# Optimization experiments

Measured on AMD Instinct MI355X. Metric: run time of the kernel, lower is better.

Reference implementation:

```python
import jax, jax.numpy as jnp
import numpy as np

N_WORDS = 8192   # total words across all concepts
L = 24           # chars per word (padded)
D = 256          # word_vec_d
H = 8            # attention heads
DFF = 1024
VOCAB = 128
N_CONCEPTS = 1024
MAXW = 16        # max_words
GROUPS = 4       # n_names: 4 equal groups of concepts


def setup_inputs() -> dict:
    key = jax.random.key(0)
    ks = jax.random.split(key, 9)
    rng = np.random.default_rng(0)
    # char tokens in [1, VOCAB), ragged word lengths in [4, L], tail = 0 (pad)
    vals = rng.integers(1, VOCAB, size=(N_WORDS, L))
    lens = rng.integers(4, L + 1, size=(N_WORDS,))
    inputs = np.where(np.arange(L)[None, :] < lens[:, None], vals, 0)
    # ragged words-per-concept: alternate 4 / 12 -> sums to N_WORDS, <= MAXW
    counts = np.where(np.arange(N_CONCEPTS) % 2 == 0, 4, 12)
    concept_id = np.repeat(np.arange(N_CONCEPTS), counts)
    word_pos = np.concatenate([np.arange(c) for c in counts])

    def w(k, shape):
        return 0.02 * jax.random.normal(k, shape, jnp.float32)

    return {
        "inputs": jnp.asarray(inputs, jnp.int32),
        "concept_id": jnp.asarray(concept_id, jnp.int32),
        "word_pos": jnp.asarray(word_pos, jnp.int32),
        "n_concepts": N_CONCEPTS,
        "n_names": GROUPS,
        "we_emb": w(ks[0], (VOCAB, D)),
        "we_qkv": w(ks[1], (D, 3 * D)),
        "we_o": w(ks[2], (D, D)),
        "we_ff1": w(ks[3], (D, DFF)),
        "we_ff2": w(ks[4], (DFF, D)),
        "ne_qkv": w(ks[5], (D, 3 * D)),
        "ne_o": w(ks[6], (D, D)),
        "ne_ff1": w(ks[7], (D, DFF)),
        "ne_ff2": w(ks[8], (DFF, D)),
    }


def _ln(x):
    m = x.mean(-1, keepdims=True)
    v = ((x - m) ** 2).mean(-1, keepdims=True)
    return (x - m) * jax.lax.rsqrt(v + 1e-5)


def _mha(x, wqkv, wo, key_pad=None):
    n, l, d = x.shape
    hd = d // H
    q, k, v = jnp.split(x @ wqkv, 3, axis=-1)
    q = q.reshape(n, l, H, hd)
    k = k.reshape(n, l, H, hd)
    v = v.reshape(n, l, H, hd)
    s = jnp.einsum('nqhd,nkhd->nhqk', q, k) / jnp.sqrt(jnp.asarray(hd, x.dtype))
    if key_pad is not None:
        s = jnp.where(key_pad[:, None, None, :], -1e9, s)
    a = jax.nn.softmax(s, axis=-1)
    o = jnp.einsum('nhqk,nkhd->nqhd', a, v).reshape(n, l, d)
    return o @ wo


def _block(x, wqkv, wo, w1, w2, key_pad=None):
    h = _ln(x + _mha(x, wqkv, wo, key_pad))
    return _ln(h + jax.nn.relu(h @ w1) @ w2)


def reference(inputs, concept_id, word_pos, n_concepts, n_names,
              we_emb, we_qkv, we_o, we_ff1, we_ff2,
              ne_qkv, ne_o, ne_ff1, ne_ff2):
    pad_mask = inputs == 0  # [N_WORDS, L]
    x = we_emb[inputs]      # [N_WORDS, L, D]
    word_ft = _block(x, we_qkv, we_o, we_ff1, we_ff2, pad_mask)
    # masked mean over chars -> one vector per word
    np_mask = (~pad_mask)[..., None].astype(word_ft.dtype)  # [N_WORDS, L, 1]
    name_vec = (word_ft * np_mask).sum(1) / np_mask.sum(1)   # [N_WORDS, D]
    # ragged -> padded: one scatter instead of per-sample torch.cat
    padded = jnp.zeros((n_concepts, MAXW, name_vec.shape[-1]), name_vec.dtype)
    padded = padded.at[concept_id, word_pos].set(name_vec)   # [n_concepts, MAXW, D]
    name_ft = _block(padded, ne_qkv, ne_o, ne_ff1, ne_ff2)
    row_pad = (padded == 0).all(-1, keepdims=True)           # all-zero rows = pad words
    name_ft = jnp.where(row_pad, jnp.zeros((), name_ft.dtype), name_ft)
    counts = (name_ft != 0).sum(1).astype(name_ft.dtype)     # [n_concepts, D]
    pooled = name_ft.sum(1) / counts                         # [n_concepts, D]
    return tuple(jnp.split(pooled, n_names, axis=0))
```

## Files before the change

### kernel.cpp

```cpp
#include <hip/hip_runtime.h>
#include <hip/hip_bf16.h>

#define NWORDS 8192
#define LW 24
#define DIM 256
#define NHEAD 8
#define DFF 1024
#define NCONC 1024
#define MAXW 16
#define TN (NCONC * MAXW)

typedef float floatx4 __attribute__((ext_vector_type(4)));
typedef short shortx8 __attribute__((ext_vector_type(8)));

__device__ __forceinline__ float bf2f(ushort u) {
  union { uint u; float f; } v; v.u = ((uint)u) << 16; return v.f;
}
__device__ __forceinline__ ushort f2bf(float f) {
  union { float f; uint u; } v; v.f = f;
  return (ushort)((v.u + 0x7FFFu + ((v.u >> 16) & 1u)) >> 16);
}

__device__ __forceinline__ void load_lds16(const ushort* gsrc, ushort* lds) {
  __builtin_amdgcn_global_load_lds((const __attribute__((address_space(1))) void*)gsrc,
                                   (__attribute__((address_space(3))) void*)lds, 16, 0, 0);
}

#define WAIT_VM0() __builtin_amdgcn_s_waitcnt(0x0F70)
#define WAIT_LGKM0() __builtin_amdgcn_s_waitcnt(0xC07F)

#define STAGE_COL(lane) ((((lane) & 3) ^ (((lane) >> 3) & 3)) * 8)
#define FRAG_OFF(row, quad) (((row) * 32) + ((((quad) ^ (((row) >> 1) & 3))) * 8))

__global__ __launch_bounds__(256) void wprep(const float* __restrict__ W,
                                             ushort* __restrict__ WT, int K, int N) {
  int idx = blockIdx.x * 256 + threadIdx.x;
  if (idx < K * N) {
    int k = idx / N, n = idx % N;
    WT[n * K + k] = f2bf(W[idx]);
  }
}

__global__ __launch_bounds__(256) void embed4(const int* __restrict__ inputs,
                                              const float* __restrict__ we_emb,
                                              ushort* __restrict__ x, int ntok) {
  int idx = blockIdx.x * 256 + threadIdx.x;
  int t = idx >> 6, d = (idx & 63) * 4;
  if (t < ntok) {
    const float4 f = *(const float4*)&we_emb[inputs[t] * DIM + d];
    uint2 o;
    o.x = (uint)f2bf(f.x) | ((uint)f2bf(f.y) << 16);
    o.y = (uint)f2bf(f.z) | ((uint)f2bf(f.w) << 16);
    *(uint2*)&x[(size_t)t * DIM + d] = o;
  }
}

template <bool LN>
__global__ __launch_bounds__(256, 2) void gemm_tok64(const ushort* __restrict__ A, int lda,
                                                     const ushort* __restrict__ BT,
                                                     const ushort* __restrict__ RES,
                                                     ushort* __restrict__ C, int ldc) {
  __shared__ __align__(16) ushort As[8 * 64 * 32];
  __shared__ __align__(16) ushort Wb[256 * 32];
  __shared__ float red1[64 * 4];
  __shared__ float red2[64 * 4];
  const int tid = threadIdx.x;
  const int w = tid >> 6, lane = tid & 63;
  const int quad = lane >> 4, l16 = lane & 15;
  const long m0 = (long)blockIdx.y * 64;
  const long nb = (long)blockIdx.x * 256;
  const int srow = lane >> 2;
  const int scol = STAGE_COL(lane);
  const int wc = w * 64;

#pragma unroll
  for (int t = 0; t < 8; t++) {
    int p = 2 * w + t / 4, ii = t % 4;
    load_lds16(&A[(m0 + ii * 16 + srow) * lda + p * 32 + scol], &As[p * 2048 + (ii * 16) * 32]);
  }
#pragma unroll
  for (int ii = 0; ii < 4; ii++)
    load_lds16(&BT[(nb + wc + ii * 16 + srow) * 256 + scol], &Wb[(wc + ii * 16) * 32]);
  __syncthreads();

  floatx4 acc[4][4] = {};
#pragma unroll 1
  for (int p = 0; p < 8; p++) {
    WAIT_VM0();
    shortx8 a[4], b[4];
#pragma unroll
    for (int j = 0; j < 4; j++)
      b[j] = *(const shortx8*)&Wb[FRAG_OFF(wc + j * 16 + l16, quad)];
    WAIT_LGKM0();
    if (p < 7) {
#pragma unroll
      for (int ii = 0; ii < 4; ii++)
        load_lds16(&BT[(nb + wc + ii * 16 + srow) * 256 + (p + 1) * 32 + scol],
                   &Wb[(wc + ii * 16) * 32]);
    }
#pragma unroll
    for (int i = 0; i < 4; i++)
      a[i] = *(const shortx8*)&As[p * 2048 + FRAG_OFF(i * 16 + l16, quad)];
#pragma unroll
    for (int i = 0; i < 4; i++)
#pragma unroll
      for (int j = 0; j < 4; j++)
        acc[i][j] = __builtin_amdgcn_mfma_f32_16x16x32_bf16(a[i], b[j], acc[i][j], 0, 0, 0);
  }

  if (!LN) {
#pragma unroll
    for (int i = 0; i < 4; i++)
#pragma unroll
      for (int j = 0; j < 4; j++)
#pragma unroll
        for (int r = 0; r < 4; r++) {
          long m = m0 + i * 16 + quad * 4 + r;
          C[m * ldc + nb + wc + j * 16 + l16] = f2bf(acc[i][j][r]);
        }
    return;
  }

#pragma unroll
  for (int i = 0; i < 4; i++)
#pragma unroll
    for (int r = 0; r < 4; r++) {
      int row = i * 16 + quad * 4 + r;
      float s1 = 0.f, s2 = 0.f;
#pragma unroll
      for (int j = 0; j < 4; j++) {
        float v = acc[i][j][r] + bf2f(RES[(m0 + row) * 256 + wc + j * 16 + l16]);
        acc[i][j][r] = v;
        s1 += v;
        s2 += v * v;
      }
#pragma unroll
      for (int off = 1; off < 16; off <<= 1) {
        s1 += __shfl_xor(s1, off);
        s2 += __shfl_xor(s2, off);
      }
      if (l16 == 0) { red1[row * 4 + w] = s1; red2[row * 4 + w] = s2; }
    }
  __syncthreads();
#pragma unroll
  for (int i = 0; i < 4; i++)
#pragma unroll
    for (int r = 0; r < 4; r++) {
      int row = i * 16 + quad * 4 + r;
      float s1 = red1[row * 4] + red1[row * 4 + 1] + red1[row * 4 + 2] + red1[row * 4 + 3];
      float s2 = red2[row * 4] + red2[row * 4 + 1] + red2[row * 4 + 2] + red2[row * 4 + 3];
      float mean = s1 * (1.f / 256.f);
      float rstd = rsqrtf(s2 * (1.f / 256.f) - mean * mean + 1e-5f);
#pragma unroll
      for (int j = 0; j < 4; j++)
        C[(m0 + row) * 256 + wc + j * 16 + l16] = f2bf((acc[i][j][r] - mean) * rstd);
    }
}

__global__ __launch_bounds__(512, 2) void ffn_fused(const ushort* __restrict__ H,
                                                    const ushort* __restrict__ W1T,
                                                    const ushort* __restrict__ W2T,
                                                    ushort* __restrict__ C,
                                                    int M) {
  __shared__ __align__(16) ushort As[8 * 128 * 32];
  __shared__ __align__(16) ushort Ss[8 * 128 * 32];
  __shared__ __align__(16) ushort Wb[256 * 32];
  const int tid = threadIdx.x;
  const int w = tid >> 6, lane = tid & 63;
  const int quad = lane >> 4, l16 = lane & 15;
  const long m0 = (long)blockIdx.x * 128;
  const int srow = lane >> 2;
  const int scol = STAGE_COL(lane);
  const int sb = w * 32;

#pragma unroll
  for (int t = 0; t < 8; t++) {
    load_lds16(&H[(m0 + t * 16 + srow) * 256 + w * 32 + scol],
               &As[w * 4096 + (t * 16) * 32]);
  }
#pragma unroll
  for (int ii = 0; ii < 2; ii++)
    load_lds16(&W1T[(long)(sb + ii * 16 + srow) * 256 + scol], &Wb[(sb + ii * 16) * 32]);
  __syncthreads();

  floatx4 acc2[8][2] = {};
  for (int m = 0; m < 4; m++) {
    floatx4 acc1[2][8] = {};
    if (m > 0) {
#pragma unroll
      for (int ii = 0; ii < 2; ii++)
        load_lds16(&W1T[(long)(m * 256 + sb + ii * 16 + srow) * 256 + scol],
                   &Wb[(sb + ii * 16) * 32]);
    }
#pragma unroll 1
    for (int p = 0; p < 8; p++) {
      WAIT_VM0();
      shortx8 a[2], b[8];
#pragma unroll
      for (int i = 0; i < 2; i++)
        a[i] = *(const shortx8*)&Wb[FRAG_OFF(sb + i * 16 + l16, quad)];
      WAIT_LGKM0();
      if (p < 7) {
#pragma unroll
        for (int ii = 0; ii < 2; ii++)
          load_lds16(&W1T[(long)(m * 256 + sb + ii * 16 + srow) * 256 + (p + 1) * 32 + scol],
                     &Wb[(sb + ii * 16) * 32]);
      }
#pragma unroll
      for (int j = 0; j < 8; j++)
        b[j] = *(const shortx8*)&As[p * 4096 + FRAG_OFF(j * 16 + l16, quad)];
#pragma unroll
      for (int i = 0; i < 2; i++)
#pragma unroll
        for (int j = 0; j < 8; j++)
          acc1[i][j] = __builtin_amdgcn_mfma_f32_16x16x32_bf16(a[i], b[j], acc1[i][j], 0, 0, 0);
    }
    __syncthreads();
#pragma unroll
    for (int i = 0; i < 2; i++) {
      int fb = sb + i * 16 + quad * 4;
      int pf = fb >> 5, c = (fb >> 3) & 3, off = fb & 7;
#pragma unroll
      for (int j = 0; j < 8; j++) {
        int tok = j * 16 + l16;
        ushort4 pk;
        pk.x = f2bf(fmaxf(acc1[i][j][0], 0.f));
        pk.y = f2bf(fmaxf(acc1[i][j][1], 0.f));
        pk.z = f2bf(fmaxf(acc1[i][j][2], 0.f));
        pk.w = f2bf(fmaxf(acc1[i][j][3], 0.f));
        *(ushort4*)&Ss[(pf * 128 + tok) * 32 + ((c ^ ((tok >> 1) & 3)) << 3) + off] = pk;
      }
    }
    __syncthreads();
#pragma unroll
    for (int jj = 0; jj < 2; jj++)
      load_lds16(&W2T[(long)(sb + jj * 16 + srow) * 1024 + m * 256 + scol],
                 &Wb[(sb + jj * 16) * 32]);
#pragma unroll 1
    for (int p = 0; p < 8; p++) {
      WAIT_VM0();
      shortx8 a[8], b[2];
#pragma unroll
      for (int j = 0; j < 2; j++)
        b[j] = *(const shortx8*)&Wb[FRAG_OFF(sb + j * 16 + l16, quad)];
      WAIT_LGKM0();
      if (p < 7) {
#pragma unroll
        for (int jj = 0; jj < 2; jj++)
          load_lds16(&W2T[(long)(sb + jj * 16 + srow) * 1024 + m * 256 + (p + 1) * 32 + scol],
                     &Wb[(sb + jj * 16) * 32]);
      }
#pragma unroll
      for (int i = 0; i < 8; i++)
        a[i] = *(const shortx8*)&Ss[p * 4096 + FRAG_OFF(i * 16 + l16, quad)];
#pragma unroll
      for (int i = 0; i < 8; i++)
#pragma unroll
        for (int j = 0; j < 2; j++)
          acc2[i][j] = __builtin_amdgcn_mfma_f32_16x16x32_bf16(a[i], b[j], acc2[i][j], 0, 0, 0);
    }
  }
  __syncthreads();

  float* red1 = (float*)Ss;
  float* red2 = red1 + 1024;
#pragma unroll
  for (int i = 0; i < 8; i++)
#pragma unroll
    for (int r = 0; r < 4; r++) {
      int row = i * 16 + quad * 4 + r;
      float s1 = 0.f, s2 = 0.f;
#pragma unroll
      for (int j = 0; j < 2; j++) {
        float v = acc2[i][j][r] + bf2f(H[(m0 + row) * 256 + sb + j * 16 + l16]);
        acc2[i][j][r] = v;
        s1 += v;
        s2 += v * v;
      }
#pragma unroll
      for (int off = 1; off < 16; off <<= 1) {
        s1 += __shfl_xor(s1, off);
        s2 += __shfl_xor(s2, off);
      }
      if (l16 == 0) { red1[row * 8 + w] = s1; red2[row * 8 + w] = s2; }
    }
  __syncthreads();
#pragma unroll
  for (int i = 0; i < 8; i++)
#pragma unroll
    for (int r = 0; r < 4; r++) {
      int row = i * 16 + quad * 4 + r;
      float s1 = 0.f, s2 = 0.f;
#pragma unroll
      for (int k = 0; k < 8; k++) { s1 += red1[row * 8 + k]; s2 += red2[row * 8 + k]; }
      float mean = s1 * (1.f / 256.f);
      float rstd = rsqrtf(s2 * (1.f / 256.f) - mean * mean + 1e-5f);
      if (m0 + row < M) {
#pragma unroll
        for (int j = 0; j < 2; j++)
          C[(m0 + row) * 256 + sb + j * 16 + l16] = f2bf((acc2[i][j][r] - mean) * rstd);
      }
    }
}

template <int LSEQ, bool MASKED>
__global__ __launch_bounds__(256) void attn(const int* __restrict__ inputs,
                                            ushort* __restrict__ qkv) {
  __shared__ ushort Qs[LSEQ * 256];
  __shared__ ushort Ks[LSEQ * 256];
  __shared__ ushort Vs[LSEQ * 256];
  __shared__ float pads[LSEQ];
  const int blk = blockIdx.x;
  const int tid = threadIdx.x;
  ushort* base = qkv + (size_t)blk * LSEQ * 768;
  const uint4* src = (const uint4*)base;
  for (int i = tid; i < LSEQ * 96; i += 256) {
    int c = i / 96, part = i % 96;
    uint4 val = src[c * 96 + part];
    int sect = part >> 5, off = part & 31;
    ushort* dst = (sect == 0) ? Qs : (sect == 1 ? Ks : Vs);
    *(uint4*)&dst[c * 256 + off * 8] = val;
  }
  if (MASKED) {
    if (tid < LSEQ) pads[tid] = (inputs[blk * LSEQ + tid] == 0) ? 1.f : 0.f;
  }
  __syncthreads();
  if (tid < LSEQ * NHEAD) {
    const int i = tid % LSEQ, hh = tid / LSEQ;
    const int hb = hh * 32;
    float q[32];
    {
      const uint4* qr = (const uint4*)&Qs[i * 256 + hb];
#pragma unroll
      for (int u = 0; u < 4; u++) {
        uint4 ch = qr[u];
        const ushort* us = (const ushort*)&ch;
#pragma unroll
        for (int d = 0; d < 8; d++) q[u * 8 + d] = bf2f(us[d]);
      }
    }
    float s[LSEQ];
    float mx = -3e38f;
#pragma unroll
    for (int j = 0; j < LSEQ; j++) {
      const uint4* kr = (const uint4*)&Ks[j * 256 + hb];
      float a = 0.f;
#pragma unroll
      for (int u = 0; u < 4; u++) {
        uint4 ch = kr[u];
        const ushort* us = (const ushort*)&ch;
#pragma unroll
        for (int d = 0; d < 8; d++) a += q[u * 8 + d] * bf2f(us[d]);
      }
      a *= 0.17677669529663687f;
      if (MASKED && pads[j] != 0.f) a = -1e9f;
      s[j] = a;
      mx = fmaxf(mx, a);
    }
    float den = 0.f;
#pragma unroll
    for (int j = 0; j < LSEQ; j++) { s[j] = __expf(s[j] - mx); den += s[j]; }
    float inv = 1.f / den;
    float o[32] = {};
#pragma unroll
    for (int j = 0; j < LSEQ; j++) {
      float a = s[j] * inv;
      const uint4* vr = (const uint4*)&Vs[j * 256 + hb];
#pragma unroll
      for (int u = 0; u < 4; u++) {
        uint4 ch = vr[u];
        const ushort* us = (const ushort*)&ch;
#pragma unroll
        for (int d = 0; d < 8; d++) o[u * 8 + d] += a * bf2f(us[d]);
      }
    }
    ushort* orow = base + (size_t)i * 768 + hb;
#pragma unroll
    for (int d = 0; d < 32; d++) orow[d] = f2bf(o[d]);
  }
}

__global__ __launch_bounds__(256) void pool_scatter(const ushort* __restrict__ ft,
                                                    const int* __restrict__ inputs,
                                                    const int* __restrict__ cid,
                                                    const int* __restrict__ wpos,
                                                    ushort* __restrict__ padded,
                                                    int* __restrict__ flags) {
  int w = blockIdx.x, d = threadIdx.x;
  float s = 0.f;
  int cnt = 0;
  for (int c = 0; c < LW; c++) {
    if (inputs[w * LW + c] != 0) {
      s += bf2f(ft[((size_t)w * LW + c) * DIM + d]);
      cnt++;
    }
  }
  int slot = cid[w] * MAXW + wpos[w];
  padded[(size_t)slot * DIM + d] = f2bf(s / (float)cnt);
  if (d == 0) flags[slot] = 1;
}

__global__ __launch_bounds__(256) void final_pool(const ushort* __restrict__ nft,
                                                  const int* __restrict__ flags,
                                                  float* __restrict__ out) {
  int n = blockIdx.x, d = threadIdx.x;
  float s = 0.f;
  int cnt = 0;
  for (int wd = 0; wd < MAXW; wd++) {
    if (flags[n * MAXW + wd]) {
      s += bf2f(nft[((size_t)n * MAXW + wd) * DIM + d]);
      cnt++;
    }
  }
  out[n * DIM + d] = s / (float)cnt;
}

extern "C" void kernel_launch(void* const* d_in, const int* in_sizes, int n_in,
                              void* d_out, int out_size, void* d_ws, size_t ws_size,
                              hipStream_t stream) {
  const int* inputs = (const int*)d_in[0];
  const int* cid = (const int*)d_in[1];
  const int* wpos = (const int*)d_in[2];
  const float* we_emb = (const float*)d_in[5];
  const float* we_qkv = (const float*)d_in[6];
  const float* we_o = (const float*)d_in[7];
  const float* we_ff1 = (const float*)d_in[8];
  const float* we_ff2 = (const float*)d_in[9];
  const float* ne_qkv = (const float*)d_in[10];
  const float* ne_o = (const float*)d_in[11];
  const float* ne_ff1 = (const float*)d_in[12];
  const float* ne_ff2 = (const float*)d_in[13];
  float* out = (float*)d_out;

  int chunks = 4;
  if (ws_size >= 515000000UL) chunks = 1;
  else if (ws_size >= 263258112UL) chunks = 2;
  const int wpc = NWORDS / chunks;
  const int tpc = wpc * LW;

  const size_t X = (size_t)tpc * DIM * 2;
  const size_t Q = (size_t)tpc * 768 * 2;

  char* base = (char*)d_ws;
  ushort* x = (ushort*)(base);
  ushort* qkv = (ushort*)(base + X);
  ushort* h = (ushort*)(base + X + Q);
  ushort* ft = qkv;
  size_t pend = X + Q + X;
  ushort* padded = (ushort*)(base + pend);
  int* flags = (int*)(base + pend + 8388608);
  ushort* wT = (ushort*)(base + pend + 8454144);
  ushort* nqkv = (ushort*)(base);
  ushort* nh = (ushort*)(base + 25165824);
  ushort* nft = (ushort*)(base + 33554432);

  ushort* wqkvT = wT;
  ushort* woT = wT + 196608;
  ushort* wff1T = wT + 262144;
  ushort* wff2T = wT + 524288;
  ushort* nqkvT = wT + 786432;
  ushort* neoT = wT + 983040;
  ushort* neff1T = wT + 1048576;
  ushort* neff2T = wT + 1310720;

  wprep<<<768, 256, 0, stream>>>(we_qkv, wqkvT, 256, 768);
  wprep<<<256, 256, 0, stream>>>(we_o, woT, 256, 256);
  wprep<<<1024, 256, 0, stream>>>(we_ff1, wff1T, 256, 1024);
  wprep<<<1024, 256, 0, stream>>>(we_ff2, wff2T, 1024, 256);
  wprep<<<768, 256, 0, stream>>>(ne_qkv, nqkvT, 256, 768);
  wprep<<<256, 256, 0, stream>>>(ne_o, neoT, 256, 256);
  wprep<<<1024, 256, 0, stream>>>(ne_ff1, neff1T, 256, 1024);
  wprep<<<1024, 256, 0, stream>>>(ne_ff2, neff2T, 1024, 256);

  (void)hipMemsetAsync(padded, 0, (size_t)TN * DIM * 2, stream);
  (void)hipMemsetAsync(flags, 0, TN * 4, stream);

  for (int c = 0; c < chunks; c++) {
    const int* in_c = inputs + (size_t)c * wpc * LW;
    const int* cid_c = cid + (size_t)c * wpc;
    const int* wpos_c = wpos + (size_t)c * wpc;

    embed4<<<tpc / 4, 256, 0, stream>>>(in_c, we_emb, x, tpc);
    {
      dim3 g(3, tpc / 64);
      gemm_tok64<false><<<g, 256, 0, stream>>>(x, 256, wqkvT, nullptr, qkv, 768);
    }
    attn<24, true><<<wpc, 256, 0, stream>>>(in_c, qkv);
    {
      dim3 g(1, tpc / 64);
      gemm_tok64<true><<<g, 256, 0, stream>>>(qkv, 768, woT, x, h, 256);
    }
    ffn_fused<<<tpc / 128, 512, 0, stream>>>(h, wff1T, wff2T, ft, tpc);
    pool_scatter<<<wpc, 256, 0, stream>>>(ft, in_c, cid_c, wpos_c, padded, flags);
  }

  {
    dim3 g(3, TN / 64);
    gemm_tok64<false><<<g, 256, 0, stream>>>(padded, 256, nqkvT, nullptr, nqkv, 768);
  }
  attn<16, false><<<NCONC, 256, 0, stream>>>(nullptr, nqkv);
  {
    dim3 g(1, TN / 64);
    gemm_tok64<true><<<g, 256, 0, stream>>>(nqkv, 768, neoT, padded, nh, 256);
  }
  ffn_fused<<<TN / 128, 512, 0, stream>>>(nh, neff1T, neff2T, nft, TN);
  final_pool<<<NCONC, 256, 0, stream>>>(nft, flags, out);
}
```

Baseline: 1.110 ms.

## Halve FFN token tile and double-buffer weight tiles across both GEMM phases

```diff
diff --git a/kernel.cpp b/kernel.cpp
--- a/kernel.cpp
+++ b/kernel.cpp
@@ -27,6 +27,7 @@
 }
 
 #define WAIT_VM0() __builtin_amdgcn_s_waitcnt(0x0F70)
+#define WAIT_VM2() __builtin_amdgcn_s_waitcnt(0x0F72)
 #define WAIT_LGKM0() __builtin_amdgcn_s_waitcnt(0xC07F)
 
 #define STAGE_COL(lane) ((((lane) & 3) ^ (((lane) >> 3) & 3)) * 8)
@@ -162,99 +163,105 @@
                                                     const ushort* __restrict__ W2T,
                                                     ushort* __restrict__ C,
                                                     int M) {
-  __shared__ __align__(16) ushort As[8 * 128 * 32];
-  __shared__ __align__(16) ushort Ss[8 * 128 * 32];
-  __shared__ __align__(16) ushort Wb[256 * 32];
+  __shared__ __align__(16) ushort As[8 * 64 * 32];
+  __shared__ __align__(16) ushort Ss[8 * 64 * 32];
+  __shared__ __align__(16) ushort Wb[2][256 * 32];
   const int tid = threadIdx.x;
   const int w = tid >> 6, lane = tid & 63;
   const int quad = lane >> 4, l16 = lane & 15;
-  const long m0 = (long)blockIdx.x * 128;
+  const long m0 = (long)blockIdx.x * 64;
   const int srow = lane >> 2;
   const int scol = STAGE_COL(lane);
   const int sb = w * 32;
 
 #pragma unroll
-  for (int t = 0; t < 8; t++) {
-    load_lds16(&H[(m0 + t * 16 + srow) * 256 + w * 32 + scol],
-               &As[w * 4096 + (t * 16) * 32]);
+  for (int t = 0; t < 4; t++) {
+    int idx = w * 4 + t, p = idx >> 2, ii = idx & 3;
+    load_lds16(&H[(m0 + ii * 16 + srow) * 256 + p * 32 + scol], &As[(p * 2048) + (ii * 16) * 32]);
   }
 #pragma unroll
   for (int ii = 0; ii < 2; ii++)
-    load_lds16(&W1T[(long)(sb + ii * 16 + srow) * 256 + scol], &Wb[(sb + ii * 16) * 32]);
+    load_lds16(&W1T[(long)(sb + ii * 16 + srow) * 256 + scol], &Wb[0][(sb + ii * 16) * 32]);
+#pragma unroll
+  for (int ii = 0; ii < 2; ii++)
+    load_lds16(&W1T[(long)(sb + ii * 16 + srow) * 256 + 32 + scol], &Wb[1][(sb + ii * 16) * 32]);
   __syncthreads();
 
-  floatx4 acc2[8][2] = {};
+  floatx4 acc2[4][2] = {};
+#pragma unroll 1
   for (int m = 0; m < 4; m++) {
-    floatx4 acc1[2][8] = {};
-    if (m > 0) {
-#pragma unroll
-      for (int ii = 0; ii < 2; ii++)
-        load_lds16(&W1T[(long)(m * 256 + sb + ii * 16 + srow) * 256 + scol],
-                   &Wb[(sb + ii * 16) * 32]);
-    }
-#pragma unroll 1
+    floatx4 acc1[2][4] = {};
+    const int mn = (m < 3) ? m + 1 : 0;
+#pragma unroll
     for (int p = 0; p < 8; p++) {
-      WAIT_VM0();
-      shortx8 a[2], b[8];
+      WAIT_VM2();
+      shortx8 a[2], b[4];
 #pragma unroll
       for (int i = 0; i < 2; i++)
-        a[i] = *(const shortx8*)&Wb[FRAG_OFF(sb + i * 16 + l16, quad)];
+        a[i] = *(const shortx8*)&Wb[p & 1][FRAG_OFF(sb + i * 16 + l16, quad)];
       WAIT_LGKM0();
-      if (p < 7) {
+      if (p < 6) {
 #pragma unroll
         for (int ii = 0; ii < 2; ii++)
-          load_lds16(&W1T[(long)(m * 256 + sb + ii * 16 + srow) * 256 + (p + 1) * 32 + scol],
-                     &Wb[(sb + ii * 16) * 32]);
-      }
-#pragma unroll
-      for (int j = 0; j < 8; j++)
-        b[j] = *(const shortx8*)&As[p * 4096 + FRAG_OFF(j * 16 + l16, quad)];
+          load_lds16(&W1T[(long)(m * 256 + sb + ii * 16 + srow) * 256 + (p + 2) * 32 + scol],
+                     &Wb[p & 1][(sb + ii * 16) * 32]);
+      } else {
+#pragma unroll
+        for (int ii = 0; ii < 2; ii++)
+          load_lds16(&W2T[(long)(sb + ii * 16 + srow) * 1024 + m * 256 + (p - 6) * 32 + scol],
+                     &Wb[p & 1][(sb + ii * 16) * 32]);
+      }
+#pragma unroll
+      for (int j = 0; j < 4; j++)
+        b[j] = *(const shortx8*)&As[p * 2048 + FRAG_OFF(j * 16 + l16, quad)];
 #pragma unroll
       for (int i = 0; i < 2; i++)
 #pragma unroll
-        for (int j = 0; j < 8; j++)
+        for (int j = 0; j < 4; j++)
           acc1[i][j] = __builtin_amdgcn_mfma_f32_16x16x32_bf16(a[i], b[j], acc1[i][j], 0, 0, 0);
     }
-    __syncthreads();
+    asm volatile("s_barrier" ::: "memory");
 #pragma unroll
     for (int i = 0; i < 2; i++) {
       int fb = sb + i * 16 + quad * 4;
       int pf = fb >> 5, c = (fb >> 3) & 3, off = fb & 7;
 #pragma unroll
-      for (int j = 0; j < 8; j++) {
+      for (int j = 0; j < 4; j++) {
         int tok = j * 16 + l16;
         ushort4 pk;
         pk.x = f2bf(fmaxf(acc1[i][j][0], 0.f));
         pk.y = f2bf(fmaxf(acc1[i][j][1], 0.f));
         pk.z = f2bf(fmaxf(acc1[i][j][2], 0.f));
         pk.w = f2bf(fmaxf(acc1[i][j][3], 0.f));
-        *(ushort4*)&Ss[(pf * 128 + tok) * 32 + ((c ^ ((tok >> 1) & 3)) << 3) + off] = pk;
-      }
-    }
-    __syncthreads();
-#pragma unroll
-    for (int jj = 0; jj < 2; jj++)
-      load_lds16(&W2T[(long)(sb + jj * 16 + srow) * 1024 + m * 256 + scol],
-                 &Wb[(sb + jj * 16) * 32]);
-#pragma unroll 1
+        *(ushort4*)&Ss[(pf * 64 + tok) * 32 + ((c ^ ((tok >> 1) & 3)) << 3) + off] = pk;
+      }
+    }
+    asm volatile("s_waitcnt lgkmcnt(0)" ::: "memory");
+    asm volatile("s_barrier" ::: "memory");
+#pragma unroll
     for (int p = 0; p < 8; p++) {
-      WAIT_VM0();
-      shortx8 a[8], b[2];
+      WAIT_VM2();
+      shortx8 a[4], b[2];
 #pragma unroll
       for (int j = 0; j < 2; j++)
-        b[j] = *(const shortx8*)&Wb[FRAG_OFF(sb + j * 16 + l16, quad)];
+        b[j] = *(const shortx8*)&Wb[p & 1][FRAG_OFF(sb + j * 16 + l16, quad)];
       WAIT_LGKM0();
-      if (p < 7) {
+      if (p < 6) {
 #pragma unroll
         for (int jj = 0; jj < 2; jj++)
-          load_lds16(&W2T[(long)(sb + jj * 16 + srow) * 1024 + m * 256 + (p + 1) * 32 + scol],
-                     &Wb[(sb + jj * 16) * 32]);
-      }
-#pragma unroll
-      for (int i = 0; i < 8; i++)
-        a[i] = *(const shortx8*)&Ss[p * 4096 + FRAG_OFF(i * 16 + l16, quad)];
-#pragma unroll
-      for (int i = 0; i < 8; i++)
+          load_lds16(&W2T[(long)(sb + jj * 16 + srow) * 1024 + m * 256 + (p + 2) * 32 + scol],
+                     &Wb[p & 1][(sb + jj * 16) * 32]);
+      } else {
+#pragma unroll
+        for (int jj = 0; jj < 2; jj++)
+          load_lds16(&W1T[(long)(mn * 256 + sb + jj * 16 + srow) * 256 + (p - 6) * 32 + scol],
+                     &Wb[p & 1][(sb + jj * 16) * 32]);
+      }
+#pragma unroll
+      for (int i = 0; i < 4; i++)
+        a[i] = *(const shortx8*)&Ss[p * 2048 + FRAG_OFF(i * 16 + l16, quad)];
+#pragma unroll
+      for (int i = 0; i < 4; i++)
 #pragma unroll
         for (int j = 0; j < 2; j++)
           acc2[i][j] = __builtin_amdgcn_mfma_f32_16x16x32_bf16(a[i], b[j], acc2[i][j], 0, 0, 0);
@@ -263,9 +270,9 @@
   __syncthreads();
 
   float* red1 = (float*)Ss;
-  float* red2 = red1 + 1024;
-#pragma unroll
-  for (int i = 0; i < 8; i++)
+  float* red2 = red1 + 512;
+#pragma unroll
+  for (int i = 0; i < 4; i++)
 #pragma unroll
     for (int r = 0; r < 4; r++) {
       int row = i * 16 + quad * 4 + r;
@@ -286,7 +293,7 @@
     }
   __syncthreads();
 #pragma unroll
-  for (int i = 0; i < 8; i++)
+  for (int i = 0; i < 4; i++)
 #pragma unroll
     for (int r = 0; r < 4; r++) {
       int row = i * 16 + quad * 4 + r;
@@ -490,7 +497,7 @@
       dim3 g(1, tpc / 64);
       gemm_tok64<true><<<g, 256, 0, stream>>>(qkv, 768, woT, x, h, 256);
     }
-    ffn_fused<<<tpc / 128, 512, 0, stream>>>(h, wff1T, wff2T, ft, tpc);
+    ffn_fused<<<tpc / 64, 512, 0, stream>>>(h, wff1T, wff2T, ft, tpc);
     pool_scatter<<<wpc, 256, 0, stream>>>(ft, in_c, cid_c, wpos_c, padded, flags);
   }
 
@@ -503,6 +510,6 @@
     dim3 g(1, TN / 64);
     gemm_tok64<true><<<g, 256, 0, stream>>>(nqkv, 768, neoT, padded, nh, 256);
   }
-  ffn_fused<<<TN / 128, 512, 0, stream>>>(nh, neff1T, neff2T, nft, TN);
+  ffn_fused<<<TN / 64, 512, 0, stream>>>(nh, neff1T, neff2T, nft, TN);
   final_pool<<<NCONC, 256, 0, stream>>>(nft, flags, out);
 }
```

Result: faster. 1.033 ms (-6.9%).
